# Performance work log

Hardware: AMD Instinct MI355X
Metric: run time of the kernel (lower is better)

Reference implementation:

```python
import jax, jax.numpy as jnp
import numpy as np


def setup_inputs() -> dict:
    key = jax.random.key(0)
    ks = jax.random.split(key, 8)
    B, N, C = 4, 2048, 1024
    H, hd, lr, R = 16, 64, 20, 200  # R = low_rank * rank_multi
    s = lambda k, shape, fan: jax.random.normal(k, shape, jnp.float32) / np.sqrt(fan)
    return {
        'x': jax.random.normal(ks[0], (B, N, C), jnp.float32),
        'qk_w': s(ks[1], (2 * C, C), C),
        'proj_w': s(ks[2], (C, C), C),
        'proj_b': jnp.zeros((C,), jnp.float32),
        'we': s(ks[3], (H, R, lr), R),
        'wr': s(ks[4], (H, R, lr), R),
        'cw_w': s(ks[5], (hd, 2 * lr), 2 * lr),
        'cw_b': jnp.zeros((hd,), jnp.float32),
    }


def _l2norm(v, eps=1e-12):
    # matches F.normalize(p=2, dim=-1): x / max(||x||, eps)
    n = jnp.sqrt(jnp.sum(v * v, axis=-1, keepdims=True))
    return v / jnp.maximum(n, eps)


def reference(x, qk_w, proj_w, proj_b, we, wr, cw_w, cw_b):
    B, N, C = x.shape
    H, R, lr = we.shape  # heads, subsample len, low_rank
    hd = C // H
    # qk projection -> q,k: [B,H,N,hd]
    qk = (x @ qk_w.T).reshape(B, N, 2, H, hd).transpose(2, 0, 3, 1, 4)
    q, k = qk[0], qk[1]
    # gen_weights: subsample N positions (embed_len > low_rank*rank_multi branch)
    idx = np.linspace(0, N - 1, R).astype(np.int64)  # static, trunc like torch
    xh = x.transpose(0, 2, 1).reshape(B, H, hd, N)[:, :, :, idx]  # [B,H,hd,R]
    we_b = jnp.einsum('bhdr,hre->bhde', xh, we)  # [B,H,hd,lr]
    wr_b = jnp.einsum('bhdr,hre->bhde', xh, wr)
    # feature map + low-rank scores
    q = _l2norm(q)
    k = _l2norm(k)
    escore = jnp.einsum('bhnd,bhde->bhne', q, we_b)  # [B,H,N,lr]
    rscore = jnp.einsum('bhnd,bhde->bhne', k, wr_b)
    score = jnp.concatenate([escore, rscore], axis=-1)  # [B,H,N,2lr]
    attn = score @ cw_w.T + cw_b  # [B,H,N,hd]
    attn = attn.transpose(0, 2, 1, 3).reshape(B, N, C)
    out = attn @ proj_w.T + proj_b  # dropout is identity at eval
    return out
```

## Files before the change

kernel.cpp:

```cpp
#include <hip/hip_runtime.h>
#include <hip/hip_bf16.h>

constexpr int B_  = 4;
constexpr int N_  = 2048;
constexpr int C_  = 1024;
constexpr int H_  = 16;
constexpr int HD  = 64;
constexpr int LR  = 20;
constexpr int RS  = 200;
constexpr int RP  = 224;

typedef __attribute__((ext_vector_type(8))) short bf16x8;
typedef __attribute__((ext_vector_type(4))) float f32x4;

__device__ __forceinline__ float b2f_raw(unsigned short u) {
    union { unsigned int i; float f; } v;
    v.i = ((unsigned int)u) << 16;
    return v.f;
}
__device__ __forceinline__ unsigned short f2b(float f) {
    __hip_bfloat16 h = __float2bfloat16(f);
    return *(unsigned short*)&h;
}

__device__ __forceinline__ void async_load16(const unsigned short* g, unsigned short* l) {
    __builtin_amdgcn_global_load_lds(
        (const __attribute__((address_space(1))) unsigned int*)(const void*)g,
        (__attribute__((address_space(3))) unsigned int*)(void*)l,
        16, 0, 0);
}

__global__ __launch_bounds__(256)
void detect_kernel(const unsigned int* __restrict__ x, int* __restrict__ flag) {
    const int t = threadIdx.x;
    int cnt = 0;
    for (int i = t; i < 1024; i += 256) {
        const unsigned int w = x[i];
        const unsigned int e = (w >> 7) & 0xFFu;
        cnt += (e >= 103u && e <= 140u) ? 1 : 0;
    }
    __shared__ int s[256];
    s[t] = cnt;
    __syncthreads();
    for (int off = 128; off > 0; off >>= 1) {
        if (t < off) s[t] += s[t + off];
        __syncthreads();
    }
    if (t == 0) *flag = (s[0] > 512) ? 1 : 0;
}

struct CvtArgs {
    const void* src[8];
    unsigned short* dst[8];
    int size[8];
};

__global__ __launch_bounds__(256)
void convert_kernel(const int* __restrict__ flag, CvtArgs args) {
    const int buf = blockIdx.y;
    const int n4 = args.size[buf] >> 2;
    const int stride = gridDim.x * blockDim.x;
    const bool isbf = (*flag != 0);
    for (int i = blockIdx.x * blockDim.x + threadIdx.x; i < n4; i += stride) {
        ushort4 o;
        if (isbf) {
            o = ((const ushort4*)args.src[buf])[i];
        } else {
            const float4 v = ((const float4*)args.src[buf])[i];
            o.x = f2b(v.x); o.y = f2b(v.y); o.z = f2b(v.z); o.w = f2b(v.w);
        }
        ((ushort4*)args.dst[buf])[i] = o;
    }
}

__global__ __launch_bounds__(256)
void gemm1_score_kernel(const unsigned short* __restrict__ xb,
                        const unsigned short* __restrict__ qkwb,
                        const unsigned short* __restrict__ we2t,
                        const unsigned short* __restrict__ wr2t,
                        const unsigned short* __restrict__ cwbb,
                        unsigned short* __restrict__ attn) {
    constexpr int BK = 32;
    constexpr int QS = 72;
    __shared__ __align__(16) unsigned short pool[2 * 128 * QS];
    unsigned short* As = pool;
    unsigned short* Bs = pool + 4096;
    unsigned short* qn = pool;
    unsigned short* kn = pool + 128 * QS;

    const int t    = threadIdx.x;
    const int wave = t >> 6;
    const int lane = t & 63;
    const int h    = blockIdx.x;
    const int m0   = blockIdx.y * 128;
    const int K    = C_;

    const int srow = lane >> 2;
    const int scol = (lane & 3) * 8;
    const unsigned short* ga0 = xb + (size_t)(m0 + wave * 16 + srow) * K + scol;
    const unsigned short* ga1 = xb + (size_t)(m0 + (wave + 4) * 16 + srow) * K + scol;
    const unsigned short* gb0 = qkwb + (size_t)(h * HD + wave * 16 + srow) * K + scol;
    const unsigned short* gb1 = qkwb + (size_t)(C_ + h * HD + wave * 16 + srow) * K + scol;
    unsigned short* lA0 = &As[wave * 512];
    unsigned short* lA1 = &As[(wave + 4) * 512];
    unsigned short* lB0 = &Bs[wave * 512];
    unsigned short* lB1 = &Bs[(wave + 4) * 512];

    const int wr = (wave >> 1) * 64;
    const int wc = (wave & 1) * 64;
    const int lq = lane >> 4;
    const int lm = lane & 15;

    f32x4 acc[4][4];
    #pragma unroll
    for (int i = 0; i < 4; ++i)
        #pragma unroll
        for (int j = 0; j < 4; ++j) acc[i][j] = 0.f;

    for (int k0 = 0; k0 < K; k0 += BK) {
        async_load16(ga0, lA0);
        async_load16(ga1, lA1);
        async_load16(gb0, lB0);
        async_load16(gb1, lB1);
        ga0 += BK; ga1 += BK; gb0 += BK; gb1 += BK;
        __syncthreads();

        bf16x8 af[4], bfr[4];
        #pragma unroll
        for (int i = 0; i < 4; ++i)
            af[i] = *(const bf16x8*)&As[(wr + i * 16 + lm) * BK + lq * 8];
        #pragma unroll
        for (int j = 0; j < 4; ++j)
            bfr[j] = *(const bf16x8*)&Bs[(wc + j * 16 + lm) * BK + lq * 8];

        #pragma unroll
        for (int i = 0; i < 4; ++i)
            #pragma unroll
            for (int j = 0; j < 4; ++j)
                acc[i][j] = __builtin_amdgcn_mfma_f32_16x16x32_bf16(
                    af[i], bfr[j], acc[i][j], 0, 0, 0);

        __syncthreads();
    }

    unsigned short* dst = (wc == 0) ? qn : kn;
    #pragma unroll
    for (int i = 0; i < 4; ++i) {
        float inv[4];
        #pragma unroll
        for (int r = 0; r < 4; ++r) {
            float s = 0.f;
            #pragma unroll
            for (int j = 0; j < 4; ++j) s += acc[i][j][r] * acc[i][j][r];
            s += __shfl_xor(s, 1, 64);
            s += __shfl_xor(s, 2, 64);
            s += __shfl_xor(s, 4, 64);
            s += __shfl_xor(s, 8, 64);
            inv[r] = 1.f / fmaxf(sqrtf(s), 1e-12f);
        }
        #pragma unroll
        for (int j = 0; j < 4; ++j)
            #pragma unroll
            for (int r = 0; r < 4; ++r) {
                const int row = wr + i * 16 + lq * 4 + r;
                dst[row * QS + j * 16 + lm] = f2b(acc[i][j][r] * inv[r]);
            }
    }
    __syncthreads();

    const int b  = blockIdx.y >> 4;
    const int bh = b * H_ + h;
    const unsigned short* wq = we2t + (size_t)bh * HD * HD;
    const unsigned short* wk = wr2t + (size_t)bh * HD * HD;

    bf16x8 bq[2][4], bk[2][4];
    #pragma unroll
    for (int t2 = 0; t2 < 2; ++t2)
        #pragma unroll
        for (int j = 0; j < 4; ++j) {
            const int dout = j * 16 + lm;
            bq[t2][j] = *(const bf16x8*)&wq[dout * HD + t2 * 32 + lq * 8];
            bk[t2][j] = *(const bf16x8*)&wk[dout * HD + t2 * 32 + lq * 8];
        }

    f32x4 accS[2][4];
    #pragma unroll
    for (int rt = 0; rt < 2; ++rt)
        #pragma unroll
        for (int j = 0; j < 4; ++j) accS[rt][j] = 0.f;

    #pragma unroll
    for (int rt = 0; rt < 2; ++rt) {
        const int lr = wave * 32 + rt * 16 + lm;
        bf16x8 aq0 = *(const bf16x8*)&qn[lr * QS + lq * 8];
        bf16x8 aq1 = *(const bf16x8*)&qn[lr * QS + 32 + lq * 8];
        bf16x8 ak0 = *(const bf16x8*)&kn[lr * QS + lq * 8];
        bf16x8 ak1 = *(const bf16x8*)&kn[lr * QS + 32 + lq * 8];
        #pragma unroll
        for (int j = 0; j < 4; ++j) {
            accS[rt][j] = __builtin_amdgcn_mfma_f32_16x16x32_bf16(aq0, bq[0][j], accS[rt][j], 0, 0, 0);
            accS[rt][j] = __builtin_amdgcn_mfma_f32_16x16x32_bf16(aq1, bq[1][j], accS[rt][j], 0, 0, 0);
            accS[rt][j] = __builtin_amdgcn_mfma_f32_16x16x32_bf16(ak0, bk[0][j], accS[rt][j], 0, 0, 0);
            accS[rt][j] = __builtin_amdgcn_mfma_f32_16x16x32_bf16(ak1, bk[1][j], accS[rt][j], 0, 0, 0);
        }
    }

    #pragma unroll
    for (int rt = 0; rt < 2; ++rt)
        #pragma unroll
        for (int j = 0; j < 4; ++j) {
            const int dout = j * 16 + lm;
            const float bv = b2f_raw(cwbb[dout]);
            #pragma unroll
            for (int r = 0; r < 4; ++r) {
                const int row = m0 + wave * 32 + rt * 16 + lq * 4 + r;
                attn[(size_t)row * C_ + h * HD + dout] = f2b(accS[rt][j][r] + bv);
            }
        }
}

template <bool OBF>
__device__ void mfma_gemm_body(const unsigned short* __restrict__ A,
                               const unsigned short* __restrict__ W,
                               const unsigned short* __restrict__ bias,
                               void* __restrict__ out,
                               int M, int N, int K) {
    constexpr int BM = 128, BN = 128, BK = 32;
    __shared__ __align__(16) unsigned short As[BM * BK];
    __shared__ __align__(16) unsigned short Bs[BN * BK];

    const int t    = threadIdx.x;
    const int wave = t >> 6;
    const int lane = t & 63;
    const int m0   = blockIdx.y * BM;
    const int n0   = blockIdx.x * BN;

    const int srow = lane >> 2;
    const int scol = (lane & 3) * 8;
    const unsigned short* ga0 = A + (size_t)(m0 + wave * 16 + srow) * K + scol;
    const unsigned short* ga1 = A + (size_t)(m0 + (wave + 4) * 16 + srow) * K + scol;
    const unsigned short* gb0 = W + (size_t)(n0 + wave * 16 + srow) * K + scol;
    const unsigned short* gb1 = W + (size_t)(n0 + (wave + 4) * 16 + srow) * K + scol;
    unsigned short* lA0 = &As[wave * 512];
    unsigned short* lA1 = &As[(wave + 4) * 512];
    unsigned short* lB0 = &Bs[wave * 512];
    unsigned short* lB1 = &Bs[(wave + 4) * 512];

    const int wr = (wave >> 1) * 64;
    const int wc = (wave & 1) * 64;
    const int lq = lane >> 4;
    const int lm = lane & 15;

    f32x4 acc[4][4];
    #pragma unroll
    for (int i = 0; i < 4; ++i)
        #pragma unroll
        for (int j = 0; j < 4; ++j) acc[i][j] = 0.f;

    for (int k0 = 0; k0 < K; k0 += BK) {
        async_load16(ga0, lA0);
        async_load16(ga1, lA1);
        async_load16(gb0, lB0);
        async_load16(gb1, lB1);
        ga0 += BK; ga1 += BK; gb0 += BK; gb1 += BK;
        __syncthreads();

        bf16x8 af[4], bfr[4];
        #pragma unroll
        for (int i = 0; i < 4; ++i)
            af[i] = *(const bf16x8*)&As[(wr + i * 16 + lm) * BK + lq * 8];
        #pragma unroll
        for (int j = 0; j < 4; ++j)
            bfr[j] = *(const bf16x8*)&Bs[(wc + j * 16 + lm) * BK + lq * 8];

        #pragma unroll
        for (int i = 0; i < 4; ++i)
            #pragma unroll
            for (int j = 0; j < 4; ++j)
                acc[i][j] = __builtin_amdgcn_mfma_f32_16x16x32_bf16(
                    af[i], bfr[j], acc[i][j], 0, 0, 0);

        __syncthreads();
    }

    #pragma unroll
    for (int i = 0; i < 4; ++i) {
        #pragma unroll
        for (int j = 0; j < 4; ++j) {
            const int col = n0 + wc + j * 16 + lm;
            const float bv = b2f_raw(bias[col]);
            #pragma unroll
            for (int r = 0; r < 4; ++r) {
                const int row = m0 + wr + i * 16 + lq * 4 + r;
                const float v = acc[i][j][r] + bv;
                if constexpr (OBF)
                    ((__hip_bfloat16*)out)[(size_t)row * N + col] = __float2bfloat16(v);
                else
                    ((float*)out)[(size_t)row * N + col] = v;
            }
        }
    }
}

__global__ __launch_bounds__(256)
void gemm2_kernel(const int* __restrict__ flag,
                  const unsigned short* __restrict__ attn,
                  const unsigned short* __restrict__ pwb,
                  const unsigned short* __restrict__ pbb,
                  void* __restrict__ out) {
    if (*flag) mfma_gemm_body<true>(attn, pwb, pbb, out, B_ * N_, C_, C_);
    else       mfma_gemm_body<false>(attn, pwb, pbb, out, B_ * N_, C_, C_);
}

__global__ __launch_bounds__(256)
void wec_kernel(const unsigned short* __restrict__ we_in,
                const unsigned short* __restrict__ wr_in,
                const unsigned short* __restrict__ cwwb,
                unsigned short* __restrict__ wect,
                unsigned short* __restrict__ wrct) {
    const int o = blockIdx.x * 256 + threadIdx.x;
    if (o >= H_ * HD * RP) return;
    const int r    = o % RP;
    const int dout = (o / RP) % HD;
    const int h    = o / (RP * HD);
    float sq = 0.f, sk = 0.f;
    if (r < RS) {
        #pragma unroll
        for (int e = 0; e < LR; ++e) {
            const float cq = b2f_raw(cwwb[dout * 2 * LR + e]);
            const float ck = b2f_raw(cwwb[dout * 2 * LR + LR + e]);
            sq += b2f_raw(we_in[((size_t)h * RS + r) * LR + e]) * cq;
            sk += b2f_raw(wr_in[((size_t)h * RS + r) * LR + e]) * ck;
        }
    }
    wect[o] = f2b(sq);
    wrct[o] = f2b(sk);
}

__global__ __launch_bounds__(256)
void gather_kernel(const unsigned short* __restrict__ xb,
                   unsigned short* __restrict__ xh) {
    const int bh = blockIdx.x;
    const int b  = bh >> 4;
    const int h  = bh & 15;
    for (int o = threadIdx.x; o < HD * RP; o += 256) {
        const int din = o & 63;
        const int r   = o >> 6;
        unsigned short v = 0;
        if (r < RS) {
            const int ir = (r * (N_ - 1)) / (RS - 1);
            v = xb[((size_t)b * N_ + ir) * C_ + h * HD + din];
        }
        xh[(size_t)bh * HD * RP + (size_t)din * RP + r] = v;
    }
}

__global__ __launch_bounds__(64)
void collapse_kernel(const unsigned short* __restrict__ xh,
                     const unsigned short* __restrict__ wect,
                     const unsigned short* __restrict__ wrct,
                     unsigned short* __restrict__ we2t,
                     unsigned short* __restrict__ wr2t) {
    const int blk = blockIdx.x;
    const int bh  = blk >> 2;
    const int qk  = (blk >> 1) & 1;
    const int dh  = blk & 1;
    const int h   = bh & 15;
    const int lane = threadIdx.x;
    const int lq = lane >> 4;
    const int lm = lane & 15;

    const unsigned short* wsrc = (qk ? wrct : wect) + (size_t)h * HD * RP;
    const unsigned short* xsrc = xh + (size_t)bh * HD * RP;
    unsigned short* dst = (qk ? wr2t : we2t) + (size_t)bh * HD * HD;

    f32x4 acc[2][4];
    #pragma unroll
    for (int i = 0; i < 2; ++i)
        #pragma unroll
        for (int j = 0; j < 4; ++j) acc[i][j] = 0.f;

    for (int ks = 0; ks < RP / 32; ++ks) {
        bf16x8 a[2], bfr[4];
        #pragma unroll
        for (int rt = 0; rt < 2; ++rt)
            a[rt] = *(const bf16x8*)&wsrc[(size_t)(dh * 32 + rt * 16 + lm) * RP + ks * 32 + lq * 8];
        #pragma unroll
        for (int j = 0; j < 4; ++j)
            bfr[j] = *(const bf16x8*)&xsrc[(size_t)(j * 16 + lm) * RP + ks * 32 + lq * 8];
        #pragma unroll
        for (int rt = 0; rt < 2; ++rt)
            #pragma unroll
            for (int j = 0; j < 4; ++j)
                acc[rt][j] = __builtin_amdgcn_mfma_f32_16x16x32_bf16(
                    a[rt], bfr[j], acc[rt][j], 0, 0, 0);
    }

    #pragma unroll
    for (int rt = 0; rt < 2; ++rt)
        #pragma unroll
        for (int j = 0; j < 4; ++j)
            #pragma unroll
            for (int r = 0; r < 4; ++r) {
                const int dout = dh * 32 + rt * 16 + lq * 4 + r;
                const int din  = j * 16 + lm;
                dst[dout * HD + din] = f2b(acc[rt][j][r]);
            }
}

extern "C" void kernel_launch(void* const* d_in, const int* in_sizes, int n_in,
                              void* d_out, int out_size, void* d_ws, size_t ws_size,
                              hipStream_t stream) {
    (void)in_sizes; (void)n_in; (void)out_size; (void)ws_size;

    char* ws = (char*)d_ws;
    size_t off = 0;
    auto alloc = [&](size_t bytes) {
        char* p = ws + off;
        off += (bytes + 255) & ~(size_t)255;
        return p;
    };

    int* flag = (int*)alloc(16);
    unsigned short* xb    = (unsigned short*)alloc((size_t)B_ * N_ * C_ * 2);
    unsigned short* qkwb  = (unsigned short*)alloc((size_t)2 * C_ * C_ * 2);
    unsigned short* pwb   = (unsigned short*)alloc((size_t)C_ * C_ * 2);
    unsigned short* pbb   = (unsigned short*)alloc((size_t)C_ * 2);
    unsigned short* we_i  = (unsigned short*)alloc((size_t)H_ * RS * LR * 2);
    unsigned short* wr_i  = (unsigned short*)alloc((size_t)H_ * RS * LR * 2);
    unsigned short* cwwb  = (unsigned short*)alloc((size_t)HD * 2 * LR * 2);
    unsigned short* cwbb  = (unsigned short*)alloc((size_t)HD * 2);
    unsigned short* attn  = (unsigned short*)alloc((size_t)B_ * N_ * C_ * 2);
    unsigned short* we2t  = (unsigned short*)alloc((size_t)B_ * H_ * HD * HD * 2);
    unsigned short* wr2t  = (unsigned short*)alloc((size_t)B_ * H_ * HD * HD * 2);
    unsigned short* wect  = (unsigned short*)alloc((size_t)H_ * HD * RP * 2);
    unsigned short* wrct  = (unsigned short*)alloc((size_t)H_ * HD * RP * 2);
    unsigned short* xh    = (unsigned short*)alloc((size_t)B_ * H_ * HD * RP * 2);

    const int M = B_ * N_;

    detect_kernel<<<1, 256, 0, stream>>>((const unsigned int*)d_in[0], flag);

    CvtArgs ca;
    ca.src[0] = d_in[0]; ca.dst[0] = xb;   ca.size[0] = B_ * N_ * C_;
    ca.src[1] = d_in[1]; ca.dst[1] = qkwb; ca.size[1] = 2 * C_ * C_;
    ca.src[2] = d_in[2]; ca.dst[2] = pwb;  ca.size[2] = C_ * C_;
    ca.src[3] = d_in[3]; ca.dst[3] = pbb;  ca.size[3] = C_;
    ca.src[4] = d_in[4]; ca.dst[4] = we_i; ca.size[4] = H_ * RS * LR;
    ca.src[5] = d_in[5]; ca.dst[5] = wr_i; ca.size[5] = H_ * RS * LR;
    ca.src[6] = d_in[6]; ca.dst[6] = cwwb; ca.size[6] = HD * 2 * LR;
    ca.src[7] = d_in[7]; ca.dst[7] = cwbb; ca.size[7] = HD;
    convert_kernel<<<dim3(2048, 8), 256, 0, stream>>>(flag, ca);

    wec_kernel<<<(H_ * HD * RP + 255) / 256, 256, 0, stream>>>(
        we_i, wr_i, cwwb, wect, wrct);
    gather_kernel<<<B_ * H_, 256, 0, stream>>>(xb, xh);
    collapse_kernel<<<B_ * H_ * 4, 64, 0, stream>>>(xh, wect, wrct, we2t, wr2t);

    gemm1_score_kernel<<<dim3(H_, M / 128), 256, 0, stream>>>(
        xb, qkwb, we2t, wr2t, cwbb, attn);

    gemm2_kernel<<<dim3(C_ / 128, M / 128), 256, 0, stream>>>(flag, attn, pwb, pbb, d_out);
}
```

Baseline: 229.5 us.

## Fuse prep kernels into one LDS-staged kernel and inline dtype detection

Replaces the separate detect, wec, gather and collapse kernels with a per-(batch,head) prep kernel. It builds the gathered x slice and the cw-collapsed weights in shared memory and runs the MFMA collapse from there. The input dtype detection now runs redundantly in every convert and gemm2 block, which removes one launch and the global flag. This cuts launch count and global round-trips for intermediates, at the cost of redundant per-block detection work and a prep stage that uses only 64 blocks.

```diff
diff --git a/kernel.cpp b/kernel.cpp
--- a/kernel.cpp
+++ b/kernel.cpp
@@ -9,6 +9,7 @@
 constexpr int LR  = 20;
 constexpr int RS  = 200;
 constexpr int RP  = 224;
+constexpr int XS  = 232;
 
 typedef __attribute__((ext_vector_type(8))) short bf16x8;
 typedef __attribute__((ext_vector_type(4))) float f32x4;
@@ -30,23 +31,25 @@
         16, 0, 0);
 }
 
-__global__ __launch_bounds__(256)
-void detect_kernel(const unsigned int* __restrict__ x, int* __restrict__ flag) {
+__device__ __forceinline__ int block_detect_flag(const unsigned int* __restrict__ xw,
+                                                 int* s ) {
     const int t = threadIdx.x;
     int cnt = 0;
-    for (int i = t; i < 1024; i += 256) {
-        const unsigned int w = x[i];
+    #pragma unroll
+    for (int i = 0; i < 4; ++i) {
+        const unsigned int w = xw[t * 4 + i];
         const unsigned int e = (w >> 7) & 0xFFu;
         cnt += (e >= 103u && e <= 140u) ? 1 : 0;
     }
-    __shared__ int s[256];
     s[t] = cnt;
     __syncthreads();
     for (int off = 128; off > 0; off >>= 1) {
         if (t < off) s[t] += s[t + off];
         __syncthreads();
     }
-    if (t == 0) *flag = (s[0] > 512) ? 1 : 0;
+    const int flag = (s[0] > 512) ? 1 : 0;
+    __syncthreads();
+    return flag;
 }
 
 struct CvtArgs {
@@ -56,11 +59,13 @@
 };
 
 __global__ __launch_bounds__(256)
-void convert_kernel(const int* __restrict__ flag, CvtArgs args) {
+void convert_kernel(CvtArgs args) {
+    __shared__ int s[256];
+    const bool isbf = (block_detect_flag((const unsigned int*)args.src[0], s) != 0);
+
     const int buf = blockIdx.y;
     const int n4 = args.size[buf] >> 2;
     const int stride = gridDim.x * blockDim.x;
-    const bool isbf = (*flag != 0);
     for (int i = blockIdx.x * blockDim.x + threadIdx.x; i < n4; i += stride) {
         ushort4 o;
         if (isbf) {
@@ -71,6 +76,104 @@
         }
         ((ushort4*)args.dst[buf])[i] = o;
     }
+}
+
+__device__ __forceinline__ void prep_fill_wcs(unsigned short* wcs,
+                                              const unsigned short* __restrict__ w_in,
+                                              const unsigned short* __restrict__ cwwb,
+                                              int h, int sel) {
+    for (int o = threadIdx.x; o < HD * RP; o += 256) {
+        const int dout = o & 63;
+        const int r    = o >> 6;
+        float s = 0.f;
+        if (r < RS) {
+            #pragma unroll
+            for (int e = 0; e < LR; ++e)
+                s += b2f_raw(w_in[((size_t)h * RS + r) * LR + e]) *
+                     b2f_raw(cwwb[dout * 2 * LR + sel * LR + e]);
+        }
+        wcs[dout * XS + r] = f2b(s);
+    }
+}
+
+__device__ __forceinline__ void prep_collapse_job(const unsigned short* wcs,
+                                                  const unsigned short* xhs,
+                                                  unsigned short* __restrict__ dst,
+                                                  int dh, int lane) {
+    const int lq = lane >> 4;
+    const int lm = lane & 15;
+    f32x4 acc[2][4];
+    #pragma unroll
+    for (int i = 0; i < 2; ++i)
+        #pragma unroll
+        for (int j = 0; j < 4; ++j) acc[i][j] = 0.f;
+
+    for (int ks = 0; ks < RP / 32; ++ks) {
+        bf16x8 a[2], bfr[4];
+        #pragma unroll
+        for (int rt = 0; rt < 2; ++rt)
+            a[rt] = *(const bf16x8*)&wcs[(dh * 32 + rt * 16 + lm) * XS + ks * 32 + lq * 8];
+        #pragma unroll
+        for (int j = 0; j < 4; ++j)
+            bfr[j] = *(const bf16x8*)&xhs[(j * 16 + lm) * XS + ks * 32 + lq * 8];
+        #pragma unroll
+        for (int rt = 0; rt < 2; ++rt)
+            #pragma unroll
+            for (int j = 0; j < 4; ++j)
+                acc[rt][j] = __builtin_amdgcn_mfma_f32_16x16x32_bf16(
+                    a[rt], bfr[j], acc[rt][j], 0, 0, 0);
+    }
+
+    #pragma unroll
+    for (int rt = 0; rt < 2; ++rt)
+        #pragma unroll
+        for (int j = 0; j < 4; ++j)
+            #pragma unroll
+            for (int r = 0; r < 4; ++r) {
+                const int dout = dh * 32 + rt * 16 + lq * 4 + r;
+                const int din  = j * 16 + lm;
+                dst[dout * HD + din] = f2b(acc[rt][j][r]);
+            }
+}
+
+__global__ __launch_bounds__(256)
+void prep_kernel(const unsigned short* __restrict__ xb,
+                 const unsigned short* __restrict__ we_in,
+                 const unsigned short* __restrict__ wr_in,
+                 const unsigned short* __restrict__ cwwb,
+                 unsigned short* __restrict__ we2t,
+                 unsigned short* __restrict__ wr2t) {
+    __shared__ __align__(16) unsigned short xhs[HD * XS];
+    __shared__ __align__(16) unsigned short wcs[HD * XS];
+
+    const int bh = blockIdx.x;
+    const int b  = bh >> 4;
+    const int h  = bh & 15;
+    const int wave = threadIdx.x >> 6;
+    const int lane = threadIdx.x & 63;
+
+    for (int o = threadIdx.x; o < HD * RP; o += 256) {
+        const int din = o & 63;
+        const int r   = o >> 6;
+        unsigned short v = 0;
+        if (r < RS) {
+            const int ir = (r * (N_ - 1)) / (RS - 1);
+            v = xb[((size_t)b * N_ + ir) * C_ + h * HD + din];
+        }
+        xhs[din * XS + r] = v;
+    }
+    prep_fill_wcs(wcs, we_in, cwwb, h, 0);
+    __syncthreads();
+
+    if (wave < 2)
+        prep_collapse_job(wcs, xhs, we2t + (size_t)bh * HD * HD, wave, lane);
+    __syncthreads();
+
+    prep_fill_wcs(wcs, wr_in, cwwb, h, 1);
+    __syncthreads();
+
+    if (wave >= 2)
+        prep_collapse_job(wcs, xhs, wr2t + (size_t)bh * HD * HD, wave - 2, lane);
 }
 
 __global__ __launch_bounds__(256)
@@ -303,109 +406,15 @@
 }
 
 __global__ __launch_bounds__(256)
-void gemm2_kernel(const int* __restrict__ flag,
+void gemm2_kernel(const unsigned int* __restrict__ x_raw,
                   const unsigned short* __restrict__ attn,
                   const unsigned short* __restrict__ pwb,
                   const unsigned short* __restrict__ pbb,
                   void* __restrict__ out) {
-    if (*flag) mfma_gemm_body<true>(attn, pwb, pbb, out, B_ * N_, C_, C_);
-    else       mfma_gemm_body<false>(attn, pwb, pbb, out, B_ * N_, C_, C_);
-}
-
-__global__ __launch_bounds__(256)
-void wec_kernel(const unsigned short* __restrict__ we_in,
-                const unsigned short* __restrict__ wr_in,
-                const unsigned short* __restrict__ cwwb,
-                unsigned short* __restrict__ wect,
-                unsigned short* __restrict__ wrct) {
-    const int o = blockIdx.x * 256 + threadIdx.x;
-    if (o >= H_ * HD * RP) return;
-    const int r    = o % RP;
-    const int dout = (o / RP) % HD;
-    const int h    = o / (RP * HD);
-    float sq = 0.f, sk = 0.f;
-    if (r < RS) {
-        #pragma unroll
-        for (int e = 0; e < LR; ++e) {
-            const float cq = b2f_raw(cwwb[dout * 2 * LR + e]);
-            const float ck = b2f_raw(cwwb[dout * 2 * LR + LR + e]);
-            sq += b2f_raw(we_in[((size_t)h * RS + r) * LR + e]) * cq;
-            sk += b2f_raw(wr_in[((size_t)h * RS + r) * LR + e]) * ck;
-        }
-    }
-    wect[o] = f2b(sq);
-    wrct[o] = f2b(sk);
-}
-
-__global__ __launch_bounds__(256)
-void gather_kernel(const unsigned short* __restrict__ xb,
-                   unsigned short* __restrict__ xh) {
-    const int bh = blockIdx.x;
-    const int b  = bh >> 4;
-    const int h  = bh & 15;
-    for (int o = threadIdx.x; o < HD * RP; o += 256) {
-        const int din = o & 63;
-        const int r   = o >> 6;
-        unsigned short v = 0;
-        if (r < RS) {
-            const int ir = (r * (N_ - 1)) / (RS - 1);
-            v = xb[((size_t)b * N_ + ir) * C_ + h * HD + din];
-        }
-        xh[(size_t)bh * HD * RP + (size_t)din * RP + r] = v;
-    }
-}
-
-__global__ __launch_bounds__(64)
-void collapse_kernel(const unsigned short* __restrict__ xh,
-                     const unsigned short* __restrict__ wect,
-                     const unsigned short* __restrict__ wrct,
-                     unsigned short* __restrict__ we2t,
-                     unsigned short* __restrict__ wr2t) {
-    const int blk = blockIdx.x;
-    const int bh  = blk >> 2;
-    const int qk  = (blk >> 1) & 1;
-    const int dh  = blk & 1;
-    const int h   = bh & 15;
-    const int lane = threadIdx.x;
-    const int lq = lane >> 4;
-    const int lm = lane & 15;
-
-    const unsigned short* wsrc = (qk ? wrct : wect) + (size_t)h * HD * RP;
-    const unsigned short* xsrc = xh + (size_t)bh * HD * RP;
-    unsigned short* dst = (qk ? wr2t : we2t) + (size_t)bh * HD * HD;
-
-    f32x4 acc[2][4];
-    #pragma unroll
-    for (int i = 0; i < 2; ++i)
-        #pragma unroll
-        for (int j = 0; j < 4; ++j) acc[i][j] = 0.f;
-
-    for (int ks = 0; ks < RP / 32; ++ks) {
-        bf16x8 a[2], bfr[4];
-        #pragma unroll
-        for (int rt = 0; rt < 2; ++rt)
-            a[rt] = *(const bf16x8*)&wsrc[(size_t)(dh * 32 + rt * 16 + lm) * RP + ks * 32 + lq * 8];
-        #pragma unroll
-        for (int j = 0; j < 4; ++j)
-            bfr[j] = *(const bf16x8*)&xsrc[(size_t)(j * 16 + lm) * RP + ks * 32 + lq * 8];
-        #pragma unroll
-        for (int rt = 0; rt < 2; ++rt)
-            #pragma unroll
-            for (int j = 0; j < 4; ++j)
-                acc[rt][j] = __builtin_amdgcn_mfma_f32_16x16x32_bf16(
-                    a[rt], bfr[j], acc[rt][j], 0, 0, 0);
-    }
-
-    #pragma unroll
-    for (int rt = 0; rt < 2; ++rt)
-        #pragma unroll
-        for (int j = 0; j < 4; ++j)
-            #pragma unroll
-            for (int r = 0; r < 4; ++r) {
-                const int dout = dh * 32 + rt * 16 + lq * 4 + r;
-                const int din  = j * 16 + lm;
-                dst[dout * HD + din] = f2b(acc[rt][j][r]);
-            }
+    __shared__ int s[256];
+    const int isbf = block_detect_flag(x_raw, s);
+    if (isbf) mfma_gemm_body<true>(attn, pwb, pbb, out, B_ * N_, C_, C_);
+    else      mfma_gemm_body<false>(attn, pwb, pbb, out, B_ * N_, C_, C_);
 }
 
 extern "C" void kernel_launch(void* const* d_in, const int* in_sizes, int n_in,
@@ -421,7 +430,6 @@
         return p;
     };
 
-    int* flag = (int*)alloc(16);
     unsigned short* xb    = (unsigned short*)alloc((size_t)B_ * N_ * C_ * 2);
     unsigned short* qkwb  = (unsigned short*)alloc((size_t)2 * C_ * C_ * 2);
     unsigned short* pwb   = (unsigned short*)alloc((size_t)C_ * C_ * 2);
@@ -433,13 +441,8 @@
     unsigned short* attn  = (unsigned short*)alloc((size_t)B_ * N_ * C_ * 2);
     unsigned short* we2t  = (unsigned short*)alloc((size_t)B_ * H_ * HD * HD * 2);
     unsigned short* wr2t  = (unsigned short*)alloc((size_t)B_ * H_ * HD * HD * 2);
-    unsigned short* wect  = (unsigned short*)alloc((size_t)H_ * HD * RP * 2);
-    unsigned short* wrct  = (unsigned short*)alloc((size_t)H_ * HD * RP * 2);
-    unsigned short* xh    = (unsigned short*)alloc((size_t)B_ * H_ * HD * RP * 2);
 
     const int M = B_ * N_;
-
-    detect_kernel<<<1, 256, 0, stream>>>((const unsigned int*)d_in[0], flag);
 
     CvtArgs ca;
     ca.src[0] = d_in[0]; ca.dst[0] = xb;   ca.size[0] = B_ * N_ * C_;
@@ -450,15 +453,13 @@
     ca.src[5] = d_in[5]; ca.dst[5] = wr_i; ca.size[5] = H_ * RS * LR;
     ca.src[6] = d_in[6]; ca.dst[6] = cwwb; ca.size[6] = HD * 2 * LR;
     ca.src[7] = d_in[7]; ca.dst[7] = cwbb; ca.size[7] = HD;
-    convert_kernel<<<dim3(2048, 8), 256, 0, stream>>>(flag, ca);
-
-    wec_kernel<<<(H_ * HD * RP + 255) / 256, 256, 0, stream>>>(
-        we_i, wr_i, cwwb, wect, wrct);
-    gather_kernel<<<B_ * H_, 256, 0, stream>>>(xb, xh);
-    collapse_kernel<<<B_ * H_ * 4, 64, 0, stream>>>(xh, wect, wrct, we2t, wr2t);
+    convert_kernel<<<dim3(2048, 8), 256, 0, stream>>>(ca);
+
+    prep_kernel<<<B_ * H_, 256, 0, stream>>>(xb, we_i, wr_i, cwwb, we2t, wr2t);
 
     gemm1_score_kernel<<<dim3(H_, M / 128), 256, 0, stream>>>(
         xb, qkwb, we2t, wr2t, cwbb, attn);
 
-    gemm2_kernel<<<dim3(C_ / 128, M / 128), 256, 0, stream>>>(flag, attn, pwb, pbb, d_out);
-}
+    gemm2_kernel<<<dim3(C_ / 128, M / 128), 256, 0, stream>>>(
+        (const unsigned int*)d_in[0], attn, pwb, pbb, d_out);
+}
```

Result: slower. 260.9 us (+13.6%).
